# Kernel tuning notes

Hardware: AMD Instinct MI355X
Metric: run time of the kernel (lower is better)

The kernel has to match this reference:

```python
import jax, jax.numpy as jnp
import numpy as np

D_MODEL = 1024
NUM_HEADS = 16
THETA = 10000.0


def _rope(x, positions):
    # x: [..., S, d_k] with interleaved even/odd pairs; positions: [S] int
    d_k = x.shape[-1]
    inv_freq = 1.0 / (THETA ** (jnp.arange(0, d_k, 2, dtype=jnp.float32) / d_k))  # [d_k/2]
    freqs = positions.astype(jnp.float32)[:, None] * inv_freq[None, :]  # [S, d_k/2]
    cos = jnp.cos(freqs)
    sin = jnp.sin(freqs)
    x_even = x[..., 0::2]
    x_odd = x[..., 1::2]
    rot_even = x_even * cos - x_odd * sin
    rot_odd = x_even * sin + x_odd * cos
    out = jnp.stack([rot_even, rot_odd], axis=-1)  # [..., S, d_k/2, 2]
    return out.reshape(x.shape)


def setup_inputs() -> dict:
    key = jax.random.key(0)
    k1, k2, k3 = jax.random.split(key, 3)
    B, S = 2, 2048
    x = jax.random.normal(k1, (B, S, D_MODEL), dtype=jnp.float32)
    Wqkv = jax.random.normal(k2, (3 * D_MODEL, D_MODEL), dtype=jnp.float32) * (D_MODEL ** -0.5)
    Wout = jax.random.normal(k3, (D_MODEL, D_MODEL), dtype=jnp.float32) * (D_MODEL ** -0.5)
    token_positions = jnp.arange(S, dtype=jnp.int32)
    return {"x": x, "Wqkv": Wqkv, "Wout": Wout, "token_positions": token_positions}


def reference(x, Wqkv, Wout, token_positions):
    B, S, D = x.shape
    H = NUM_HEADS
    d_k = D // H
    qkv = x @ Wqkv.T  # [B, S, 3D]
    qkv = qkv.reshape(B, S, 3, H, d_k).transpose(0, 2, 3, 1, 4)  # [B, 3, H, S, d_k]
    q, k, v = qkv[:, 0], qkv[:, 1], qkv[:, 2]  # each [B, H, S, d_k]
    q = _rope(q, token_positions)
    k = _rope(k, token_positions)
    scores = jnp.einsum("bhqd,bhkd->bhqk", q, k) / jnp.sqrt(jnp.float32(d_k))
    attn = jax.nn.softmax(scores, axis=-1)
    out = jnp.einsum("bhqk,bhkd->bhqd", attn, v)  # [B, H, S, d_k]
    out = out.transpose(0, 2, 1, 3).reshape(B, S, D)
    return out @ Wout.T
```

## Files before the change

### kernel.cpp

```cpp
#include <hip/hip_runtime.h>
#include <stdint.h>

typedef unsigned short u16;
typedef unsigned int u32;
typedef __bf16 bf16x8 __attribute__((ext_vector_type(8)));
typedef float f32x4 __attribute__((ext_vector_type(4)));
typedef float f32x16 __attribute__((ext_vector_type(16)));

#define MFMA16 __builtin_amdgcn_mfma_f32_16x16x32_bf16
#define MFMA32 __builtin_amdgcn_mfma_f32_32x32x16_bf16

static __device__ __forceinline__ u16 f2bf(float f) {
  union { float f; u32 u; } v; v.f = f;
  u32 r = v.u + 0x7FFFu + ((v.u >> 16) & 1u);
  return (u16)(r >> 16);
}
static __device__ __forceinline__ float bf2f(u16 b) {
  union { float f; u32 u; } v; v.u = ((u32)b) << 16;
  return v.f;
}
static __device__ __forceinline__ void load_lds16(const void* g, void* l) {
  __builtin_amdgcn_global_load_lds(
      (const __attribute__((address_space(1))) void*)g,
      (__attribute__((address_space(3))) void*)l, 16, 0, 0);
}

__global__ __launch_bounds__(256) void cvt_bf16(const float* __restrict__ in,
                                                u16* __restrict__ out, int n4) {
  int i = blockIdx.x * 256 + threadIdx.x;
  if (i >= n4) return;
  float4 v = reinterpret_cast<const float4*>(in)[i];
  uint2 r;
  r.x = (u32)f2bf(v.x) | ((u32)f2bf(v.y) << 16);
  r.y = (u32)f2bf(v.z) | ((u32)f2bf(v.w) << 16);
  reinterpret_cast<uint2*>(out)[i] = r;
}

template <bool OUT_BF16>
__global__ __launch_bounds__(256, 2) void gemm_bt(const u16* __restrict__ A,
                                                  const u16* __restrict__ B,
                                                  void* __restrict__ Cv,
                                                  int M, int N, int K) {
  __shared__ u16 As[128 * 32];
  __shared__ u16 Bs[128 * 32];
  const int t = threadIdx.x;
  const int w = t >> 6, lane = t & 63;
  const int brow = blockIdx.y * 128, bcol = blockIdx.x * 128;
  const int wr = (w >> 1) * 64, wc = (w & 1) * 64;

  f32x4 acc[4][4];
#pragma unroll
  for (int i = 0; i < 4; ++i)
#pragma unroll
    for (int j = 0; j < 4; ++j) acc[i][j] = (f32x4){0.f, 0.f, 0.f, 0.f};

  const int srow = w * 16 + (lane >> 2);
  const int scol = (lane & 3) * 8;
  const u16* ga = A + (size_t)(brow + srow) * K + scol;
  const u16* gb = B + (size_t)(bcol + srow) * K + scol;
  const size_t rstep = (size_t)64 * K;
  u16* ldsA = As + w * 512;
  u16* ldsB = Bs + w * 512;

  const int lc = lane & 15, lg = lane >> 4;
  const int kg = lg * 8;

  const int nk = K >> 5;
  for (int kt = 0; kt < nk; ++kt) {
    __syncthreads();
    load_lds16(ga, ldsA);
    load_lds16(ga + rstep, (char*)ldsA + 4096);
    load_lds16(gb, ldsB);
    load_lds16(gb + rstep, (char*)ldsB + 4096);
    ga += 32; gb += 32;
    asm volatile("s_waitcnt vmcnt(0)" ::: "memory");
    __syncthreads();
    bf16x8 af[4], bfr[4];
#pragma unroll
    for (int i = 0; i < 4; ++i)
      af[i] = *reinterpret_cast<const bf16x8*>(As + (wr + i * 16 + lc) * 32 + kg);
#pragma unroll
    for (int j = 0; j < 4; ++j)
      bfr[j] = *reinterpret_cast<const bf16x8*>(Bs + (wc + j * 16 + lc) * 32 + kg);
#pragma unroll
    for (int i = 0; i < 4; ++i)
#pragma unroll
      for (int j = 0; j < 4; ++j)
        acc[i][j] = MFMA16(af[i], bfr[j], acc[i][j], 0, 0, 0);
  }

  const int r0 = lg * 4;
#pragma unroll
  for (int i = 0; i < 4; ++i)
#pragma unroll
    for (int j = 0; j < 4; ++j)
#pragma unroll
      for (int r = 0; r < 4; ++r) {
        const int m = brow + wr + i * 16 + r0 + r;
        const int n = bcol + wc + j * 16 + lc;
        if constexpr (OUT_BF16)
          ((u16*)Cv)[(size_t)m * N + n] = f2bf(acc[i][j][r]);
        else
          ((float*)Cv)[(size_t)m * N + n] = acc[i][j][r];
      }
}

__global__ __launch_bounds__(256) void build_trig(const int* __restrict__ pos,
                                                  float2* __restrict__ tab) {
  int i = blockIdx.x * 256 + threadIdx.x;
  int s = i >> 5, p = i & 31;
  float inv = powf(10000.0f, -(float)p * (1.0f / 32.0f));
  float fr = (float)pos[s] * inv;
  float sn, cs;
  sincosf(fr, &sn, &cs);
  tab[i] = make_float2(cs, sn);
}

__global__ __launch_bounds__(256) void rope_repack(const u16* __restrict__ qkv,
                                                   const float2* __restrict__ tab,
                                                   u16* __restrict__ Qro,
                                                   u16* __restrict__ Kro) {
  int idx = blockIdx.x * 256 + threadIdx.x;
  int p = idx & 31;
  int h = (idx >> 5) & 15;
  int m = idx >> 9;
  int b = m >> 11, s = m & 2047;
  const u32* row = reinterpret_cast<const u32*>(qkv + (size_t)m * 3072);
  u32 qp = row[h * 32 + p];
  u32 kp = row[512 + h * 32 + p];
  float2 cssn = tab[s * 32 + p];
  float cs = cssn.x, sn = cssn.y;
  float qe = bf2f((u16)(qp & 0xffffu)), qo = bf2f((u16)(qp >> 16));
  float ke = bf2f((u16)(kp & 0xffffu)), ko = bf2f((u16)(kp >> 16));
  const float QS = 0.18033688011112042f;
  float qre = (qe * cs - qo * sn) * QS;
  float qro_ = (qe * sn + qo * cs) * QS;
  float kre = ke * cs - ko * sn;
  float kro_ = ke * sn + ko * cs;
  size_t o = ((size_t)(b * 16 + h) * 2048 + s) * 32 + p;
  reinterpret_cast<u32*>(Qro)[o] = (u32)f2bf(qre) | ((u32)f2bf(qro_) << 16);
  reinterpret_cast<u32*>(Kro)[o] = (u32)f2bf(kre) | ((u32)f2bf(kro_) << 16);
}

__global__ __launch_bounds__(256) void v_transpose(const u16* __restrict__ qkv,
                                                   u16* __restrict__ VT) {
  const int bh = blockIdx.y;
  const int s0 = blockIdx.x * 64;
  const int b = bh >> 4, h = bh & 15;
  __shared__ u16 tile[64][72];
  const int t = threadIdx.x;
#pragma unroll
  for (int c = 0; c < 2; ++c) {
    int r = c * 32 + (t >> 3);
    int d = (t & 7) * 8;
    const u16* src = qkv + (size_t)(b * 2048 + s0 + r) * 3072 + 2048 + h * 64 + d;
    *reinterpret_cast<uint4*>(&tile[r][d]) = *reinterpret_cast<const uint4*>(src);
  }
  __syncthreads();
#pragma unroll
  for (int c = 0; c < 2; ++c) {
    int dd = c * 32 + (t >> 3);
    int sg = (t & 7) * 8;
    u16 tmp[8];
#pragma unroll
    for (int jj = 0; jj < 8; ++jj) tmp[jj] = tile[sg + jj][dd];
    *reinterpret_cast<uint4*>(VT + ((size_t)bh * 64 + dd) * 2048 + s0 + sg) =
        *reinterpret_cast<const uint4*>(tmp);
  }
}


static __device__ __forceinline__ void qk_tile(const char* lk,
                                               const bf16x8 (&qf)[4],
                                               f32x16 (&S)[2], int l31, int hi) {
#pragma unroll
  for (int i = 0; i < 2; ++i)
#pragma unroll
    for (int r = 0; r < 16; ++r) S[i][r] = 0.f;
  __builtin_amdgcn_s_setprio(1);
#pragma unroll
  for (int d = 0; d < 4; ++d) {
#pragma unroll
    for (int kvt = 0; kvt < 2; ++kvt) {
      int kv = kvt * 32 + l31;
      int a = (kv * 128 + d * 32 + hi * 16) ^ ((kv & 7) << 4);
      bf16x8 kf = *reinterpret_cast<const bf16x8*>(lk + a);
      S[kvt] = MFMA32(kf, qf[d], S[kvt], 0, 0, 0);
    }
  }
  __builtin_amdgcn_s_setprio(0);
}

static __device__ __forceinline__ void sm_pv(const char* lv, f32x16 (&SA)[2],
                                             f32x16 (&Oacc)[2], float& m,
                                             float& lsum, int l31, int hi) {
  float mt[16];
#pragma unroll
  for (int r = 0; r < 16; ++r) mt[r] = fmaxf(SA[0][r], SA[1][r]);
#pragma unroll
  for (int d = 8; d >= 1; d >>= 1)
#pragma unroll
    for (int r = 0; r < d; ++r) mt[r] = fmaxf(mt[r], mt[r + d]);
  float pmax = fmaxf(mt[0], __shfl_xor(mt[0], 32));

  if (__any(pmax > m + 6.0f)) {
    float mn = fmaxf(m, pmax);
    float sc = exp2f(m - mn);
    m = mn;
    lsum *= sc;
#pragma unroll
    for (int i = 0; i < 2; ++i)
#pragma unroll
      for (int r = 0; r < 16; ++r) Oacc[i][r] *= sc;
  }

#pragma unroll
  for (int kvt = 0; kvt < 2; ++kvt)
#pragma unroll
    for (int r = 0; r < 16; ++r) SA[kvt][r] = exp2f(SA[kvt][r] - m);

  {
    float st[16];
#pragma unroll
    for (int r = 0; r < 16; ++r) st[r] = SA[0][r] + SA[1][r];
#pragma unroll
    for (int d = 8; d >= 1; d >>= 1)
#pragma unroll
      for (int r = 0; r < d; ++r) st[r] += st[r + d];
    lsum += st[0];
  }

  bf16x8 pfrag[4];
#pragma unroll
  for (int kvt = 0; kvt < 2; ++kvt)
#pragma unroll
    for (int s1 = 0; s1 < 2; ++s1) {
      u32 X0, X1, Y0, Y1;
      const int c0 = s1 * 8, c1 = c0 + 4;
      asm("v_cvt_pk_bf16_f32 %0, %1, %2"
          : "=v"(X0) : "v"(SA[kvt][c0 + 0]), "v"(SA[kvt][c0 + 1]));
      asm("v_cvt_pk_bf16_f32 %0, %1, %2"
          : "=v"(X1) : "v"(SA[kvt][c0 + 2]), "v"(SA[kvt][c0 + 3]));
      asm("v_cvt_pk_bf16_f32 %0, %1, %2"
          : "=v"(Y0) : "v"(SA[kvt][c1 + 0]), "v"(SA[kvt][c1 + 1]));
      asm("v_cvt_pk_bf16_f32 %0, %1, %2"
          : "=v"(Y1) : "v"(SA[kvt][c1 + 2]), "v"(SA[kvt][c1 + 3]));
      asm("v_permlane32_swap_b32 %0, %1" : "+v"(X0), "+v"(Y0));
      asm("v_permlane32_swap_b32 %0, %1" : "+v"(X1), "+v"(Y1));
      union { u32 w[4]; bf16x8 v; } u;
      u.w[0] = X0; u.w[1] = X1; u.w[2] = Y0; u.w[3] = Y1;
      pfrag[kvt * 2 + s1] = u.v;
    }

  __builtin_amdgcn_s_setprio(1);
#pragma unroll
  for (int s = 0; s < 4; ++s) {
#pragma unroll
    for (int dt = 0; dt < 2; ++dt) {
      int d = dt * 32 + l31;
      int a = (d * 128 + s * 32 + hi * 16) ^ ((d & 7) << 4);
      bf16x8 vf = *reinterpret_cast<const bf16x8*>(lv + a);
      Oacc[dt] = MFMA32(vf, pfrag[s], Oacc[dt], 0, 0, 0);
    }
  }
  __builtin_amdgcn_s_setprio(0);
}

__global__ __launch_bounds__(256) void attn_fwd2(const u16* __restrict__ Q,
                                                 const u16* __restrict__ Kg,
                                                 const u16* __restrict__ VTg,
                                                 u16* __restrict__ O) {
  constexpr int S = 2048, NT = 32;
  __shared__ char lds[4][16384];
  const int t = threadIdx.x, wv = t >> 6, lane = t & 63;
  const int bid = blockIdx.x;
  const int slot = bid >> 3;
  const int bh = (bid & 7) * 4 + (slot >> 4);
  const int qb = slot & 15;
  const int b = bh >> 4, h = bh & 15;
  const int q0 = qb * 128 + wv * 32;
  const size_t kbase = (size_t)bh * (S * 64);
  const int l31 = lane & 31, hi = lane >> 5;

  bf16x8 qf[4];
  {
    const u16* qp = Q + kbase + (size_t)(q0 + l31) * 64 + hi * 8;
#pragma unroll
    for (int d = 0; d < 4; ++d)
      qf[d] = *reinterpret_cast<const bf16x8*>(qp + d * 16);
  }

  f32x16 Oacc[2];
#pragma unroll
  for (int i = 0; i < 2; ++i)
#pragma unroll
    for (int r = 0; r < 16; ++r) Oacc[i][r] = 0.f;
  float m = -__builtin_inff(), lsum = 0.f;

  const char* gk0 = (const char*)(Kg + kbase);
  const char* gv0 = (const char*)(VTg + kbase);

#define STAGE(KT, BUF)                                                         \
  {                                                                            \
    char* lk_ = lds[BUF];                                                      \
    const char* gk_ = gk0 + (size_t)(KT) * 8192;                               \
    _Pragma("unroll") for (int c_ = 0; c_ < 2; ++c_) {                         \
      int o_ = (c_ * 256 + t) * 16;                                            \
      int row_ = o_ >> 7, colb_ = o_ & 127;                                    \
      int swz_ = colb_ ^ ((row_ & 7) << 4);                                    \
      load_lds16(gk_ + row_ * 128 + swz_, lk_ + o_);                           \
      load_lds16(gv0 + (size_t)row_ * 4096 + (KT) * 128 + swz_,                \
                 lk_ + 8192 + o_);                                             \
    }                                                                          \
  }

#define HALF(T, SA, SB, DO_QK)                                                 \
  {                                                                            \
    asm volatile("s_waitcnt vmcnt(4)" ::: "memory");                           \
    __builtin_amdgcn_s_barrier();                                              \
    int st_ = (T) + 3 < NT ? (T) + 3 : NT - 1;                                 \
    STAGE(st_, ((T) + 3) & 3)                                                  \
    if (DO_QK) qk_tile(lds[((T) + 1) & 3], qf, SB, l31, hi);                   \
    sm_pv(lds[(T) & 3] + 8192, SA, Oacc, m, lsum, l31, hi);                    \
  }

  f32x16 SaA[2], SaB[2];

  STAGE(0, 0)
  STAGE(1, 1)
  STAGE(2, 2)
  asm volatile("s_waitcnt vmcnt(8)" ::: "memory");
  __builtin_amdgcn_s_barrier();
  qk_tile(lds[0], qf, SaA, l31, hi);

  for (int u = 0; u < 15; ++u) {
    const int t0 = 2 * u;
    HALF(t0, SaA, SaB, true)
    HALF(t0 + 1, SaB, SaA, true)
  }
  HALF(30, SaA, SaB, true)
  HALF(31, SaB, SaA, false)
#undef HALF
#undef STAGE

  const float lfull = lsum + __shfl_xor(lsum, 32);
  const float rdiv = 1.0f / lfull;
  const int srow = q0 + l31;
  u16* orow = O + (size_t)(b * S + srow) * 1024 + h * 64;
#pragma unroll
  for (int dt = 0; dt < 2; ++dt)
#pragma unroll
    for (int c = 0; c < 4; ++c) {
      float v0 = Oacc[dt][4 * c + 0] * rdiv;
      float v1 = Oacc[dt][4 * c + 1] * rdiv;
      float v2 = Oacc[dt][4 * c + 2] * rdiv;
      float v3 = Oacc[dt][4 * c + 3] * rdiv;
      uint2 pk;
      pk.x = (u32)f2bf(v0) | ((u32)f2bf(v1) << 16);
      pk.y = (u32)f2bf(v2) | ((u32)f2bf(v3) << 16);
      *reinterpret_cast<uint2*>(orow + dt * 32 + c * 8 + hi * 4) = pk;
    }
}

extern "C" void kernel_launch(void* const* d_in, const int* in_sizes, int n_in,
                              void* d_out, int out_size, void* d_ws, size_t ws_size,
                              hipStream_t stream) {
  (void)in_sizes; (void)n_in; (void)out_size; (void)ws_size;
  const float* x = (const float*)d_in[0];
  const float* wqkv = (const float*)d_in[1];
  const float* wout = (const float*)d_in[2];
  const int* pos = (const int*)d_in[3];
  float* out = (float*)d_out;

  char* ws = (char*)d_ws;
  u16* xb     = (u16*)(ws);
  u16* wqkvb  = (u16*)(ws + 8388608);
  u16* woutb  = (u16*)(ws + 14680064);
  u16* qkvb   = (u16*)(ws + 16777216);
  u16* qro    = (u16*)(ws + 41943040);
  u16* kro    = (u16*)(ws + 50331648);
  u16* vt     = (u16*)(ws + 58720256);
  u16* attno  = (u16*)(ws + 67108864);
  float2* tab = (float2*)(ws + 75497472);

  cvt_bf16<<<4096, 256, 0, stream>>>(x, xb, 1048576);
  cvt_bf16<<<3072, 256, 0, stream>>>(wqkv, wqkvb, 786432);
  cvt_bf16<<<1024, 256, 0, stream>>>(wout, woutb, 262144);
  build_trig<<<256, 256, 0, stream>>>(pos, tab);
  gemm_bt<true><<<dim3(24, 32), 256, 0, stream>>>(xb, wqkvb, qkvb, 4096, 3072, 1024);
  rope_repack<<<8192, 256, 0, stream>>>(qkvb, tab, qro, kro);
  v_transpose<<<dim3(32, 32), 256, 0, stream>>>(qkvb, vt);
  attn_fwd2<<<512, 256, 0, stream>>>(qro, kro, vt, attno);
  gemm_bt<false><<<dim3(8, 32), 256, 0, stream>>>(attno, woutb, out, 4096, 1024, 1024);
}
```

Measured before the change: 230.7 us.

## Split attention KV range into two partials with a separate merge kernel

The attention kernel now splits each query block's KV sequence into two halves processed by separate workgroups, doubling the grid to 1024 blocks. Unnormalized bf16 partial outputs plus (sum, max) stats are written out, and a new merge kernel rescales and combines them. The software pipeline also shrinks from a 4-buffer, 3-deep prefetch with overlapped QK/PV to a simple double buffer with a full vmcnt(0) wait each iteration, while launch bounds request higher occupancy. The extra launch, partial-result traffic and loss of deep prefetching may outweigh the gain in parallelism, since 512 blocks already exceeds the CU count. Partials are stored in bf16 before normalization, which adds rounding error.

```diff
diff --git a/kernel.cpp b/kernel.cpp
--- a/kernel.cpp
+++ b/kernel.cpp
@@ -266,18 +266,19 @@
   __builtin_amdgcn_s_setprio(0);
 }
 
-__global__ __launch_bounds__(256) void attn_fwd2(const u16* __restrict__ Q,
-                                                 const u16* __restrict__ Kg,
-                                                 const u16* __restrict__ VTg,
-                                                 u16* __restrict__ O) {
-  constexpr int S = 2048, NT = 32;
-  __shared__ char lds[4][16384];
+__global__ __launch_bounds__(256, 4) void attn_split(const u16* __restrict__ Q,
+                                                     const u16* __restrict__ Kg,
+                                                     const u16* __restrict__ VTg,
+                                                     u16* __restrict__ part,
+                                                     float2* __restrict__ stats) {
+  constexpr int S = 2048, NT = 16;
+  __shared__ char lds[2][16384];
   const int t = threadIdx.x, wv = t >> 6, lane = t & 63;
   const int bid = blockIdx.x;
   const int slot = bid >> 3;
-  const int bh = (bid & 7) * 4 + (slot >> 4);
-  const int qb = slot & 15;
-  const int b = bh >> 4, h = bh & 15;
+  const int bh = (bid & 7) * 4 + (slot >> 5);
+  const int rest = slot & 31;
+  const int qb = rest >> 1, sp = rest & 1;
   const int q0 = qb * 128 + wv * 32;
   const size_t kbase = (size_t)bh * (S * 64);
   const int l31 = lane & 31, hi = lane >> 5;
@@ -303,63 +304,71 @@
 #define STAGE(KT, BUF)                                                         \
   {                                                                            \
     char* lk_ = lds[BUF];                                                      \
-    const char* gk_ = gk0 + (size_t)(KT) * 8192;                               \
+    const char* gk_ = gk0 + (size_t)(sp * 16 + (KT)) * 8192;                   \
     _Pragma("unroll") for (int c_ = 0; c_ < 2; ++c_) {                         \
       int o_ = (c_ * 256 + t) * 16;                                            \
       int row_ = o_ >> 7, colb_ = o_ & 127;                                    \
       int swz_ = colb_ ^ ((row_ & 7) << 4);                                    \
       load_lds16(gk_ + row_ * 128 + swz_, lk_ + o_);                           \
-      load_lds16(gv0 + (size_t)row_ * 4096 + (KT) * 128 + swz_,                \
+      load_lds16(gv0 + (size_t)row_ * 4096 + sp * 2048 + (KT) * 128 + swz_,    \
                  lk_ + 8192 + o_);                                             \
     }                                                                          \
   }
 
-#define HALF(T, SA, SB, DO_QK)                                                 \
-  {                                                                            \
-    asm volatile("s_waitcnt vmcnt(4)" ::: "memory");                           \
-    __builtin_amdgcn_s_barrier();                                              \
-    int st_ = (T) + 3 < NT ? (T) + 3 : NT - 1;                                 \
-    STAGE(st_, ((T) + 3) & 3)                                                  \
-    if (DO_QK) qk_tile(lds[((T) + 1) & 3], qf, SB, l31, hi);                   \
-    sm_pv(lds[(T) & 3] + 8192, SA, Oacc, m, lsum, l31, hi);                    \
-  }
-
-  f32x16 SaA[2], SaB[2];
-
   STAGE(0, 0)
-  STAGE(1, 1)
-  STAGE(2, 2)
-  asm volatile("s_waitcnt vmcnt(8)" ::: "memory");
-  __builtin_amdgcn_s_barrier();
-  qk_tile(lds[0], qf, SaA, l31, hi);
-
-  for (int u = 0; u < 15; ++u) {
-    const int t0 = 2 * u;
-    HALF(t0, SaA, SaB, true)
-    HALF(t0 + 1, SaB, SaA, true)
-  }
-  HALF(30, SaA, SaB, true)
-  HALF(31, SaB, SaA, false)
-#undef HALF
+
+  f32x16 Sa[2];
+  for (int kt = 0; kt < NT; ++kt) {
+    asm volatile("s_waitcnt vmcnt(0)" ::: "memory");
+    __builtin_amdgcn_s_barrier();
+    if (kt + 1 < NT) STAGE(kt + 1, (kt + 1) & 1)
+    const char* lb = lds[kt & 1];
+    qk_tile(lb, qf, Sa, l31, hi);
+    sm_pv(lb + 8192, Sa, Oacc, m, lsum, l31, hi);
+  }
 #undef STAGE
 
   const float lfull = lsum + __shfl_xor(lsum, 32);
-  const float rdiv = 1.0f / lfull;
   const int srow = q0 + l31;
-  u16* orow = O + (size_t)(b * S + srow) * 1024 + h * 64;
+  const size_t rowi = (size_t)(sp * 32 + bh) * 2048 + srow;
+  u16* prow = part + rowi * 64;
 #pragma unroll
   for (int dt = 0; dt < 2; ++dt)
 #pragma unroll
     for (int c = 0; c < 4; ++c) {
-      float v0 = Oacc[dt][4 * c + 0] * rdiv;
-      float v1 = Oacc[dt][4 * c + 1] * rdiv;
-      float v2 = Oacc[dt][4 * c + 2] * rdiv;
-      float v3 = Oacc[dt][4 * c + 3] * rdiv;
       uint2 pk;
-      pk.x = (u32)f2bf(v0) | ((u32)f2bf(v1) << 16);
-      pk.y = (u32)f2bf(v2) | ((u32)f2bf(v3) << 16);
-      *reinterpret_cast<uint2*>(orow + dt * 32 + c * 8 + hi * 4) = pk;
+      pk.x = (u32)f2bf(Oacc[dt][4 * c + 0]) | ((u32)f2bf(Oacc[dt][4 * c + 1]) << 16);
+      pk.y = (u32)f2bf(Oacc[dt][4 * c + 2]) | ((u32)f2bf(Oacc[dt][4 * c + 3]) << 16);
+      *reinterpret_cast<uint2*>(prow + dt * 32 + c * 8 + hi * 4) = pk;
     }
+  if (hi == 0) stats[rowi] = make_float2(lfull, m);
+}
+
+__global__ __launch_bounds__(256) void attn_merge(const u16* __restrict__ part,
+                                                  const float2* __restrict__ stats,
+                                                  u16* __restrict__ attno) {
+  int idx = blockIdx.x * 256 + threadIdx.x;
+  int r = idx >> 3, c = idx & 7;
+  float2 s0 = stats[r];
+  float2 s1 = stats[65536 + r];
+  float M = fmaxf(s0.y, s1.y);
+  float w0 = exp2f(s0.y - M), w1 = exp2f(s1.y - M);
+  float rden = 1.0f / (w0 * s0.x + w1 * s1.x);
+  w0 *= rden; w1 *= rden;
+  const uint4 a = *reinterpret_cast<const uint4*>(part + (size_t)r * 64 + c * 8);
+  const uint4 b4 = *reinterpret_cast<const uint4*>(part + 4194304 + (size_t)r * 64 + c * 8);
+  const u32 aw[4] = {a.x, a.y, a.z, a.w}, bw[4] = {b4.x, b4.y, b4.z, b4.w};
+  u32 ow[4];
+#pragma unroll
+  for (int i = 0; i < 4; ++i) {
+    float r0 = w0 * bf2f((u16)(aw[i] & 0xffffu)) + w1 * bf2f((u16)(bw[i] & 0xffffu));
+    float r1 = w0 * bf2f((u16)(aw[i] >> 16)) + w1 * bf2f((u16)(bw[i] >> 16));
+    ow[i] = (u32)f2bf(r0) | ((u32)f2bf(r1) << 16);
+  }
+  int bh = r >> 11, s = r & 2047;
+  int b = bh >> 4, h = bh & 15;
+  uint4 o; o.x = ow[0]; o.y = ow[1]; o.z = ow[2]; o.w = ow[3];
+  *reinterpret_cast<uint4*>(attno + (size_t)(b * 2048 + s) * 1024 + h * 64 + c * 8) = o;
 }
 
 extern "C" void kernel_launch(void* const* d_in, const int* in_sizes, int n_in,
@@ -383,6 +392,9 @@
   u16* attno  = (u16*)(ws + 67108864);
   float2* tab = (float2*)(ws + 75497472);
 
+  u16* part     = qkvb;
+  float2* stats = (float2*)(ws + 16777216 + 16777216);
+
   cvt_bf16<<<4096, 256, 0, stream>>>(x, xb, 1048576);
   cvt_bf16<<<3072, 256, 0, stream>>>(wqkv, wqkvb, 786432);
   cvt_bf16<<<1024, 256, 0, stream>>>(wout, woutb, 262144);
@@ -390,6 +402,7 @@
   gemm_bt<true><<<dim3(24, 32), 256, 0, stream>>>(xb, wqkvb, qkvb, 4096, 3072, 1024);
   rope_repack<<<8192, 256, 0, stream>>>(qkvb, tab, qro, kro);
   v_transpose<<<dim3(32, 32), 256, 0, stream>>>(qkvb, vt);
-  attn_fwd2<<<512, 256, 0, stream>>>(qro, kro, vt, attno);
+  attn_split<<<1024, 256, 0, stream>>>(qro, kro, vt, part, stats);
+  attn_merge<<<2048, 256, 0, stream>>>(part, stats, attno);
   gemm_bt<false><<<dim3(8, 32), 256, 0, stream>>>(attno, woutb, out, 4096, 1024, 1024);
 }
```

Result: faster. 224.1 us (-2.8%).
